# Performance work log

Measured on AMD Instinct MI355X. Metric: run time of the kernel, lower is better.

Reference implementation:

```python
import jax, jax.numpy as jnp
import numpy as np

B, NA, LAT, HID, AF, L = 512, 58, 64, 128, 10, 2
N = B * NA
E = N * 16


def silu(x):
    return x * jax.nn.sigmoid(x)


def setup_inputs() -> dict:
    key = jax.random.key(0)
    ks = list(jax.random.split(key, 32))

    def p(k, shape, fan_in):
        return jax.random.normal(k, shape, jnp.float32) / np.sqrt(fan_in)

    inp = {
        "z": jax.random.normal(ks[0], (B, LAT), jnp.float32),
        "atom_types": jax.random.uniform(ks[1], (N, AF), jnp.float32),
        "edge_index": jax.random.randint(ks[2], (2, E), 0, N, jnp.int64),
        "init_coords": jax.random.normal(ks[3], (NA, 3), jnp.float32) * 0.1,
        "latent_w": p(ks[4], (LAT, HID), LAT), "latent_b": jnp.zeros((HID,), jnp.float32),
        "atom_w": p(ks[5], (AF, HID), AF), "atom_b": jnp.zeros((HID,), jnp.float32),
        # per-layer stacked params (leading dim = num_layers)
        "edge_w1": p(ks[6], (L, 2 * HID + 1, HID), 2 * HID + 1), "edge_b1": jnp.zeros((L, HID), jnp.float32),
        "edge_w2": p(ks[7], (L, HID, HID), HID), "edge_b2": jnp.zeros((L, HID), jnp.float32),
        "node_w1": p(ks[8], (L, 2 * HID, HID), 2 * HID), "node_b1": jnp.zeros((L, HID), jnp.float32),
        "node_w2": p(ks[9], (L, HID, HID), HID), "node_b2": jnp.zeros((L, HID), jnp.float32),
        "coord_w1": p(ks[10], (L, HID, HID), HID), "coord_b1": jnp.zeros((L, HID), jnp.float32),
        "coord_w2": p(ks[11], (L, HID, 1), HID),  # no bias
        "ln_g": jnp.ones((L, HID), jnp.float32), "ln_b": jnp.zeros((L, HID), jnp.float32),
        "head_w1": p(ks[12], (HID, HID // 2), HID), "head_b1": jnp.zeros((HID // 2,), jnp.float32),
        "head_w2": p(ks[13], (HID // 2, 3), HID // 2), "head_b2": jnp.zeros((3,), jnp.float32),
    }
    return inp


def _layer(h, pos, row, col, ew1, eb1, ew2, eb2, nw1, nb1, nw2, nb2, cw1, cb1, cw2, lg, lb):
    n = h.shape[0]
    xi, xj = h[row], h[col]                      # [E,HID] gathers
    rel = pos[row] - pos[col]                    # [E,3]
    d2 = jnp.clip(jnp.sum(rel * rel, axis=-1, keepdims=True), 1e-6, 1e6)
    ef = jnp.concatenate([xi, xj, d2], axis=-1)  # [E,2H+1]
    m = silu(silu(ef @ ew1 + eb1) @ ew2 + eb2)   # edge MLP messages [E,HID]
    agg = jax.ops.segment_sum(m, row, num_segments=n)
    hn = silu(jnp.concatenate([h, agg], axis=-1) @ nw1 + nb1) @ nw2 + nb2
    mu = jnp.mean(hn, axis=-1, keepdims=True)
    var = jnp.mean((hn - mu) ** 2, axis=-1, keepdims=True)
    hn = (hn - mu) * jax.lax.rsqrt(var + 1e-5) * lg + lb
    cw = jnp.clip(silu(m @ cw1 + cb1) @ cw2, -1.0, 1.0)  # [E,1]
    upd = jax.ops.segment_sum(cw * rel, row, num_segments=n)  # [N,3]
    deg = jax.ops.segment_sum(jnp.ones((row.shape[0],), pos.dtype), row, num_segments=n)[:, None]
    pos_new = pos + upd / (deg + 1e-6)
    return hn, pos_new


def reference(z, atom_types, edge_index, init_coords, latent_w, latent_b, atom_w, atom_b,
              edge_w1, edge_b1, edge_w2, edge_b2, node_w1, node_b1, node_w2, node_b2,
              coord_w1, coord_b1, coord_w2, ln_g, ln_b, head_w1, head_b1, head_w2, head_b2):
    b = z.shape[0]
    na = init_coords.shape[0]
    n = b * na
    h = z @ latent_w + latent_b                              # [B,HID]
    h = jnp.broadcast_to(h[:, None, :], (b, na, h.shape[-1])).reshape(n, -1)
    h = h + (atom_types @ atom_w + atom_b)
    pos = jnp.broadcast_to(init_coords[None], (b, na, 3)).reshape(n, 3)
    row, col = edge_index[0], edge_index[1]
    for l in range(edge_w1.shape[0]):
        h, pos = _layer(h, pos, row, col,
                        edge_w1[l], edge_b1[l], edge_w2[l], edge_b2[l],
                        node_w1[l], node_b1[l], node_w2[l], node_b2[l],
                        coord_w1[l], coord_b1[l], coord_w2[l], ln_g[l], ln_b[l])
    delta = silu(h @ head_w1 + head_b1) @ head_w2 + head_b2
    return pos + delta
```

## Files before the change

kernel.cpp:

```cpp
#include <hip/hip_runtime.h>
#include <hip/hip_bf16.h>

#define BB 512
#define NA 58
#define LAT 64
#define HID 128
#define AF 10
#define NL 2
#define NN (BB*NA)
#define NE (NN*16)
#define ET 64
#define NTILE (NE/ET)

typedef __attribute__((ext_vector_type(8))) short s8;
typedef __attribute__((ext_vector_type(4))) float f4;

struct CvtDesc {
    const void* src[24];
    float*      dst[24];
    int         len[24];
};

struct PackJobs {
    const float* src[11];
    short*       dst[11];
    int          K[11];
    int          mode[11];
};

__device__ __forceinline__ float siluf(float x) {
    return x * __builtin_amdgcn_rcpf(1.0f + __expf(-x));
}

__device__ __forceinline__ short f2b(float x) {
    __hip_bfloat16 b = __float2bfloat16(x);
    return *(short*)&b;
}

__device__ __forceinline__ float b2f(short s) {
    return __uint_as_float(((unsigned int)(unsigned short)s) << 16);
}

__global__ void k_detect(const unsigned short* __restrict__ z16,
                         const unsigned int* __restrict__ e32,
                         int* __restrict__ flags) {
    __shared__ int sbf, si64;
    if (threadIdx.x == 0) { sbf = 0; si64 = 0; }
    __syncthreads();
    int c1 = 0, c2 = 0;
    for (int i = threadIdx.x; i < 1024; i += 256) {
        unsigned short v = z16[2*i];
        int e = (v >> 7) & 0xFF;
        if (e >= 100 && e <= 140) c1++;
        if (e32[2*i + 1] == 0u) c2++;
    }
    atomicAdd(&sbf, c1);
    atomicAdd(&si64, c2);
    __syncthreads();
    if (threadIdx.x == 0) {
        flags[0] = (sbf  > 600) ? 1 : 0;
        flags[1] = (si64 > 600) ? 1 : 0;
    }
}

__global__ void k_convert(CvtDesc d, const int* __restrict__ flags) {
    int a = blockIdx.y;
    int i = blockIdx.x * blockDim.x + threadIdx.x;
    int n = d.len[a];
    if (i >= n) return;
    if (flags[0]) {
        d.dst[a][i] = __bfloat162float(((const __hip_bfloat16*)d.src[a])[i]);
    } else {
        d.dst[a][i] = ((const float*)d.src[a])[i];
    }
}

__global__ void k_packall(PackJobs pj) {
    int j = blockIdx.y;
    int idx = blockIdx.x * 256 + threadIdx.x;
    const float* w = pj.src[j];
    short* o = pj.dst[j];
    int mode = pj.mode[j];
    if (mode == 0) {
        int K = pj.K[j];
        if (idx >= 128*K) return;
        int jj = idx & 7;
        int l  = (idx >> 3) & 63;
        int rest = idx >> 9;
        int KC = K >> 5;
        int kc = rest % KC;
        int nt = rest / KC;
        int n = nt*16 + (l & 15);
        int k = kc*32 + (l >> 4)*8 + jj;
        o[idx] = f2b(w[k*128 + n]);
    } else if (mode == 1) {
        if (idx >= 32768) return;
        int jj = idx & 7;
        int l  = (idx >> 3) & 63;
        int rest = idx >> 9;
        int kc = rest & 3;
        int nt = rest >> 2;
        int n = nt*16 + (l & 15);
        int k = kc*32 + (l >> 4)*8 + jj;
        float v = (n < 128) ? w[k*128 + n] : w[(128 + k)*128 + (n - 128)];
        o[idx] = f2b(v);
    } else {
        if (idx >= 8192) return;
        int jj = idx & 7;
        int l  = (idx >> 3) & 63;
        int rest = idx >> 9;
        int kc = rest & 3;
        int nt = rest >> 2;
        int n = nt*16 + (l & 15);
        int k = kc*32 + (l >> 4)*8 + jj;
        o[idx] = f2b(w[k*64 + n]);
    }
}

__global__ void k_hist(const int* __restrict__ eidx, const int* __restrict__ flags,
                       int* __restrict__ cnt) {
    int e = blockIdx.x * 256 + threadIdx.x;
    if (e >= NE) return;
    int is64 = flags[1];
    int r = eidx[is64 ? 2*(long)e : (long)e];
    atomicAdd(&cnt[r], 1);
}

__global__ __launch_bounds__(1024) void k_scan(const int* __restrict__ cnt,
                                               int* __restrict__ rowStart,
                                               int* __restrict__ cursor) {
    __shared__ int part[1024];
    int t = threadIdx.x;
    int base = t * 29;
    int loc[29];
    int s = 0;
    #pragma unroll
    for (int i = 0; i < 29; ++i) { loc[i] = s; s += cnt[base + i]; }
    part[t] = s;
    __syncthreads();
    for (int d = 1; d < 1024; d <<= 1) {
        int v = (t >= d) ? part[t - d] : 0;
        __syncthreads();
        part[t] += v;
        __syncthreads();
    }
    int pre = (t == 0) ? 0 : part[t - 1];
    #pragma unroll
    for (int i = 0; i < 29; ++i) {
        int v = pre + loc[i];
        rowStart[base + i] = v;
        cursor[base + i] = v;
    }
    if (t == 1023) rowStart[NN] = pre + s;
}

__global__ void k_scatter(const int* __restrict__ eidx, const int* __restrict__ flags,
                          int* __restrict__ cursor,
                          int* __restrict__ rS, int* __restrict__ cS) {
    int e = blockIdx.x * 256 + threadIdx.x;
    if (e >= NE) return;
    int is64 = flags[1];
    long ge = e, gc = (long)e + NE;
    int r = eidx[is64 ? 2*ge : ge];
    int c = eidx[is64 ? 2*gc : gc];
    int p = atomicAdd(&cursor[r], 1);
    rS[p] = r; cS[p] = c;
}

__global__ __launch_bounds__(256) void k_init3(
    const float* __restrict__ z, const float* __restrict__ lw,
    const float* __restrict__ lbz,
    const float* __restrict__ at,
    const float* __restrict__ aw, const float* __restrict__ ab,
    const float* __restrict__ ic,
    float* __restrict__ pos, short* __restrict__ hb,
    const short* __restrict__ wcat0, const float* __restrict__ b10,
    short* __restrict__ H1, float* __restrict__ agg, float* __restrict__ upd)
{
    __shared__ short x[64][136];
    __shared__ float awS[AF][HID];
    __shared__ float atS[64][AF+2];
    __shared__ float zbS[3][LAT];
    __shared__ float hzS[3][HID];
    const int tid = threadIdx.x;
    const int n0 = blockIdx.x * 64;
    const int b0 = n0 / NA;
    const int nb = (n0 + 63) / NA - b0 + 1;

    for (int i = tid; i < AF*HID; i += 256) awS[i/HID][i%HID] = aw[i];
    for (int i = tid; i < 64*AF; i += 256)
        atS[i/AF][i%AF] = at[(long)(n0 + i/AF)*AF + i%AF];
    for (int i = tid; i < nb*LAT; i += 256) {
        int bi = i / LAT, k = i - bi*LAT;
        int bidx = b0 + bi;
        zbS[bi][k] = (bidx < BB) ? z[bidx*LAT + k] : 0.f;
    }
    __syncthreads();

    for (int i = tid; i < nb*HID; i += 256) {
        int bi = i / HID, c = i - bi*HID;
        float acc = lbz[c];
        #pragma unroll
        for (int k = 0; k < LAT; ++k) acc += zbS[bi][k] * lw[k*HID + c];
        hzS[bi][c] = acc;
    }
    __syncthreads();

    #pragma unroll
    for (int it = 0; it < 32; ++it) {
        int idx = it*256 + tid;
        int r = idx >> 7, c = idx & 127;
        int n = n0 + r;
        float v = hzS[n/NA - b0][c] + ab[c];
        #pragma unroll
        for (int f = 0; f < AF; ++f) v += atS[r][f]*awS[f][c];
        short s = f2b(v);
        x[r][c] = s;
        hb[(long)n*HID + c] = s;
    }
    if (tid < 192) {
        int i = tid/3, d = tid - i*3;
        int n = n0 + i;
        pos[n*3 + d] = ic[(n % NA)*3 + d];
        upd[n*3 + d] = 0.f;
    }
    {
        f4* a4 = (f4*)(agg + (long)n0*HID);
        for (int j = tid; j < 64*HID/4; j += 256) a4[j] = (f4)0.f;
    }
    __syncthreads();

    const int l = tid & 63, w = tid >> 6;
    const int l16 = l & 15, quad = l >> 4;
    f4 acc[4][4];
    #pragma unroll
    for (int mt = 0; mt < 4; ++mt)
        #pragma unroll
        for (int nt4 = 0; nt4 < 4; ++nt4) acc[mt][nt4] = (f4)0.f;
    #pragma unroll
    for (int kc = 0; kc < 4; ++kc) {
        s8 a[4];
        #pragma unroll
        for (int mt = 0; mt < 4; ++mt)
            a[mt] = *(const s8*)&x[mt*16 + l16][kc*32 + quad*8];
        #pragma unroll
        for (int nt4 = 0; nt4 < 4; ++nt4) {
            int nt = w*4 + nt4;
            s8 b = *(const s8*)(wcat0 + (((size_t)nt*4 + kc)*64 + l)*8);
            #pragma unroll
            for (int mt = 0; mt < 4; ++mt)
                acc[mt][nt4] = __builtin_amdgcn_mfma_f32_16x16x32_bf16(a[mt], b, acc[mt][nt4], 0, 0, 0);
        }
    }
    #pragma unroll
    for (int nt4 = 0; nt4 < 4; ++nt4) {
        int col = (w*4 + nt4)*16 + l16;
        float bias = (col < 128) ? b10[col] : 0.f;
        #pragma unroll
        for (int mt = 0; mt < 4; ++mt)
            #pragma unroll
            for (int i = 0; i < 4; ++i) {
                int row = mt*16 + quad*4 + i;
                H1[(long)(n0 + row)*256 + col] = f2b(acc[mt][nt4][i] + bias);
            }
    }
}

__global__ __launch_bounds__(256, 3) void k_edge_os(
    const short* __restrict__ H1,
    const int* __restrict__ rS, const int* __restrict__ cS,
    const float* __restrict__ pos,
    const float* __restrict__ w1c,
    const short* __restrict__ w2p, const float* __restrict__ b2,
    const short* __restrict__ c1p, const float* __restrict__ cb1,
    const float* __restrict__ cw2,
    float* __restrict__ agg, float* __restrict__ upd)
{
    __shared__ short t1[ET][136];
    __shared__ short mm[ET][136];
    __shared__ int   rIs[ET], cIs[ET];
    __shared__ float sred[ET];

    const int tid = threadIdx.x;
    const int l = tid & 63, w = tid >> 6;
    const int l16 = l & 15, quad = l >> 4;
    const int c0 = (2*w)*16 + l16, c1c = (2*w+1)*16 + l16;
    const int half = tid >> 7, ch = tid & 127;
    const int q = tid & 15;
    const int esub = tid >> 4;
    const int T = blockIdx.x;

    float wv[8];
    #pragma unroll
    for (int j = 0; j < 8; ++j) wv[j] = w1c[q*8 + j];

    s8 w2f[8], c1f[8];
    #pragma unroll
    for (int kc = 0; kc < 4; ++kc) {
        w2f[kc]     = *(const s8*)(w2p + (((size_t)(2*w)*4 + kc)*64 + l)*8);
        w2f[4 + kc] = *(const s8*)(w2p + (((size_t)(2*w+1)*4 + kc)*64 + l)*8);
        c1f[kc]     = *(const s8*)(c1p + (((size_t)(2*w)*4 + kc)*64 + l)*8);
        c1f[4 + kc] = *(const s8*)(c1p + (((size_t)(2*w+1)*4 + kc)*64 + l)*8);
    }
    const float bia2_0 = b2[c0],  bia2_1 = b2[c1c];
    const float biac_0 = cb1[c0], biac_1 = cb1[c1c];
    const float cw0    = cw2[c0], cw1v   = cw2[c1c];

    const long eb = (long)T * ET;
    if (tid < ET) sred[tid] = 0.f;
    #pragma unroll
    for (int it = 0; it < 4; ++it) {
        int e = esub + 16*it;
        int r = rS[eb + e], c = cS[eb + e];
        float rx = pos[r*3+0] - pos[c*3+0];
        float ry = pos[r*3+1] - pos[c*3+1];
        float rz = pos[r*3+2] - pos[c*3+2];
        float d2 = fminf(fmaxf(rx*rx + ry*ry + rz*rz, 1e-6f), 1e6f);
        s8 va = *(const s8*)(H1 + (long)r*256 + q*8);
        s8 vb = *(const s8*)(H1 + (long)c*256 + 128 + q*8);
        s8 o;
        #pragma unroll
        for (int j = 0; j < 8; ++j)
            o[j] = f2b(siluf(b2f(va[j]) + b2f(vb[j]) + d2*wv[j]));
        *(s8*)&t1[e][q*8] = o;
        if (q == 0) { rIs[e] = r; cIs[e] = c; }
    }
    __syncthreads();

    {
        f4 acc[4][2];
        #pragma unroll
        for (int mt = 0; mt < 4; ++mt) { acc[mt][0] = (f4)0.f; acc[mt][1] = (f4)0.f; }
        #pragma unroll
        for (int it = 0; it < 4; ++it) {
            #pragma unroll
            for (int mt = 0; mt < 4; ++mt) {
                s8 a = *(const s8*)&t1[mt*16 + l16][it*32 + quad*8];
                acc[mt][0] = __builtin_amdgcn_mfma_f32_16x16x32_bf16(a, w2f[it],     acc[mt][0], 0, 0, 0);
                acc[mt][1] = __builtin_amdgcn_mfma_f32_16x16x32_bf16(a, w2f[4 + it], acc[mt][1], 0, 0, 0);
            }
        }
        #pragma unroll
        for (int mt = 0; mt < 4; ++mt) {
            #pragma unroll
            for (int i = 0; i < 4; ++i) {
                int row = mt*16 + quad*4 + i;
                mm[row][c0]  = f2b(siluf(acc[mt][0][i] + bia2_0));
                mm[row][c1c] = f2b(siluf(acc[mt][1][i] + bia2_1));
            }
        }
    }
    __syncthreads();

    {
        int e0 = half * 32;
        int cur = rIs[e0];
        float a = 0.f;
        #pragma unroll
        for (int e = e0; e < e0 + 32; ++e) {
            int r = rIs[e];
            if (r != cur) {
                atomicAdd(&agg[(long)cur*HID + ch], a);
                a = 0.f; cur = r;
            }
            a += b2f(mm[e][ch]);
        }
        atomicAdd(&agg[(long)cur*HID + ch], a);
    }
    {
        f4 acc3[4][2];
        #pragma unroll
        for (int mt = 0; mt < 4; ++mt) { acc3[mt][0] = (f4)0.f; acc3[mt][1] = (f4)0.f; }
        #pragma unroll
        for (int kc = 0; kc < 4; ++kc) {
            #pragma unroll
            for (int mt = 0; mt < 4; ++mt) {
                s8 a = *(const s8*)&mm[mt*16 + l16][kc*32 + quad*8];
                acc3[mt][0] = __builtin_amdgcn_mfma_f32_16x16x32_bf16(a, c1f[kc],     acc3[mt][0], 0, 0, 0);
                acc3[mt][1] = __builtin_amdgcn_mfma_f32_16x16x32_bf16(a, c1f[4 + kc], acc3[mt][1], 0, 0, 0);
            }
        }
        #pragma unroll
        for (int mt = 0; mt < 4; ++mt) {
            #pragma unroll
            for (int i = 0; i < 4; ++i) {
                float p = siluf(acc3[mt][0][i] + biac_0) * cw0
                        + siluf(acc3[mt][1][i] + biac_1) * cw1v;
                p += __shfl_xor(p, 1);
                p += __shfl_xor(p, 2);
                p += __shfl_xor(p, 4);
                p += __shfl_xor(p, 8);
                if (l16 == 0) {
                    int row = mt*16 + quad*4 + i;
                    atomicAdd(&sred[row], p);
                }
            }
        }
    }
    int   ur = 0;
    float urx = 0.f, ury = 0.f, urz = 0.f;
    if (tid < ET) {
        ur = rIs[tid];
        int uc = cIs[tid];
        urx = pos[ur*3+0] - pos[uc*3+0];
        ury = pos[ur*3+1] - pos[uc*3+1];
        urz = pos[ur*3+2] - pos[uc*3+2];
    }
    __syncthreads();

    if (tid < ET) {
        float cwv = fminf(fmaxf(sred[tid], -1.f), 1.f);
        atomicAdd(&upd[ur*3+0], cwv*urx);
        atomicAdd(&upd[ur*3+1], cwv*ury);
        atomicAdd(&upd[ur*3+2], cwv*urz);
    }
}

__global__ __launch_bounds__(256) void k_node_mfma(
    short* __restrict__ hb, float* __restrict__ agg,
    const short* __restrict__ w1p, const float* __restrict__ b1n,
    const short* __restrict__ w2p, const float* __restrict__ b2n,
    const float* __restrict__ lg, const float* __restrict__ lb,
    float* __restrict__ pos, float* __restrict__ upd,
    const int* __restrict__ rowStart,
    const short* __restrict__ wcatn, const float* __restrict__ b1next,
    short* __restrict__ H1,
    const short* __restrict__ hw1p, const float* __restrict__ hb1,
    const float* __restrict__ hw2, const float* __restrict__ hb2,
    void* __restrict__ out, const int* __restrict__ flags)
{
    __shared__ short x[64][264];
    __shared__ short t1[64][144];
    __shared__ float mus[64], rstds[64];
    __shared__ float posS[64][3];
    float (*hn)[132] = (float (*)[132])&x[0][0];
    float (*hid)[68] = (float (*)[68])&x[0][0];

    const int tid = threadIdx.x;
    const int n0 = blockIdx.x * 64;

    #pragma unroll
    for (int it = 0; it < 4; ++it) {
        int idx = it*256 + tid;
        int e = idx >> 4, qq = idx & 15;
        *(int4*)&x[e][qq*8] = *(const int4*)(hb + (long)(n0+e)*HID + qq*8);
    }
    #pragma unroll
    for (int it = 0; it < 8; ++it) {
        int idx = it*256 + tid;
        int e = idx >> 5, qq = idx & 31;
        float4 v = *(const float4*)(agg + (long)(n0+e)*HID + qq*4);
        short4 sv;
        sv.x = f2b(v.x); sv.y = f2b(v.y); sv.z = f2b(v.z); sv.w = f2b(v.w);
        *(short4*)&x[e][128 + qq*4] = sv;
    }
    __syncthreads();

    {
        f4* a4 = (f4*)(agg + (long)n0*HID);
        for (int j = tid; j < 64*HID/4; j += 256) a4[j] = (f4)0.f;
    }

    const int l = tid & 63, w = tid >> 6;
    const int l16 = l & 15, quad = l >> 4;
    const int nt0 = 2*w, nt1 = 2*w + 1;
    const int c0 = nt0*16 + l16, c1c = nt1*16 + l16;

    {
        f4 acc[4][2];
        #pragma unroll
        for (int mt = 0; mt < 4; ++mt) { acc[mt][0] = (f4)0.f; acc[mt][1] = (f4)0.f; }
        #pragma unroll
        for (int kc = 0; kc < 8; ++kc) {
            s8 b0  = *(const s8*)(w1p + (((size_t)nt0*8 + kc)*64 + l)*8);
            s8 b1f = *(const s8*)(w1p + (((size_t)nt1*8 + kc)*64 + l)*8);
            #pragma unroll
            for (int mt = 0; mt < 4; ++mt) {
                s8 a = *(const s8*)&x[mt*16 + l16][kc*32 + quad*8];
                acc[mt][0] = __builtin_amdgcn_mfma_f32_16x16x32_bf16(a, b0,  acc[mt][0], 0, 0, 0);
                acc[mt][1] = __builtin_amdgcn_mfma_f32_16x16x32_bf16(a, b1f, acc[mt][1], 0, 0, 0);
            }
        }
        float bia0 = b1n[c0], bia1 = b1n[c1c];
        #pragma unroll
        for (int mt = 0; mt < 4; ++mt) {
            #pragma unroll
            for (int i = 0; i < 4; ++i) {
                int row = mt*16 + quad*4 + i;
                t1[row][c0]  = f2b(siluf(acc[mt][0][i] + bia0));
                t1[row][c1c] = f2b(siluf(acc[mt][1][i] + bia1));
            }
        }
    }
    __syncthreads();

    {
        f4 acc[4][2];
        #pragma unroll
        for (int mt = 0; mt < 4; ++mt) { acc[mt][0] = (f4)0.f; acc[mt][1] = (f4)0.f; }
        #pragma unroll
        for (int kc = 0; kc < 4; ++kc) {
            s8 b0  = *(const s8*)(w2p + (((size_t)nt0*4 + kc)*64 + l)*8);
            s8 b1f = *(const s8*)(w2p + (((size_t)nt1*4 + kc)*64 + l)*8);
            #pragma unroll
            for (int mt = 0; mt < 4; ++mt) {
                s8 a = *(const s8*)&t1[mt*16 + l16][kc*32 + quad*8];
                acc[mt][0] = __builtin_amdgcn_mfma_f32_16x16x32_bf16(a, b0,  acc[mt][0], 0, 0, 0);
                acc[mt][1] = __builtin_amdgcn_mfma_f32_16x16x32_bf16(a, b1f, acc[mt][1], 0, 0, 0);
            }
        }
        float bia0 = b2n[c0], bia1 = b2n[c1c];
        __syncthreads();
        #pragma unroll
        for (int mt = 0; mt < 4; ++mt) {
            #pragma unroll
            for (int i = 0; i < 4; ++i) {
                int row = mt*16 + quad*4 + i;
                hn[row][c0]  = acc[mt][0][i] + bia0;
                hn[row][c1c] = acc[mt][1][i] + bia1;
            }
        }
    }
    __syncthreads();

    {
        int r = tid >> 2, part = tid & 3;
        float s = 0.f, qv = 0.f;
        #pragma unroll
        for (int j = 0; j < 32; ++j) {
            float v = hn[r][part + 4*j];
            s += v; qv += v*v;
        }
        s += __shfl_xor(s, 1); qv += __shfl_xor(qv, 1);
        s += __shfl_xor(s, 2); qv += __shfl_xor(qv, 2);
        if (part == 0) {
            float mu = s * (1.0f/HID);
            float var = qv * (1.0f/HID) - mu*mu;
            mus[r] = mu;
            rstds[r] = rsqrtf(var + 1e-5f);
        }
    }
    __syncthreads();

    #pragma unroll
    for (int it = 0; it < 32; ++it) {
        int idx = it*256 + tid;
        int r = idx >> 7, c = idx & 127;
        float v = (hn[r][c] - mus[r]) * rstds[r] * lg[c] + lb[c];
        short s = f2b(v);
        hb[(long)(n0 + r)*HID + c] = s;
        t1[r][c] = s;
    }
    if (tid < 192) {
        int i = tid / 3, d = tid - i*3;
        int n = n0 + i;
        float dg = (float)(rowStart[n+1] - rowStart[n]);
        float np = pos[n*3+d] + upd[n*3+d] / (dg + 1e-6f);
        pos[n*3+d] = np;
        posS[i][d] = np;
        upd[n*3+d] = 0.f;
    }
    __syncthreads();

    if (wcatn) {
        f4 acc[4][4];
        #pragma unroll
        for (int mt = 0; mt < 4; ++mt)
            #pragma unroll
            for (int nt4 = 0; nt4 < 4; ++nt4) acc[mt][nt4] = (f4)0.f;
        #pragma unroll
        for (int kc = 0; kc < 4; ++kc) {
            s8 a[4];
            #pragma unroll
            for (int mt = 0; mt < 4; ++mt)
                a[mt] = *(const s8*)&t1[mt*16 + l16][kc*32 + quad*8];
            #pragma unroll
            for (int nt4 = 0; nt4 < 4; ++nt4) {
                int nt = w*4 + nt4;
                s8 b = *(const s8*)(wcatn + (((size_t)nt*4 + kc)*64 + l)*8);
                #pragma unroll
                for (int mt = 0; mt < 4; ++mt)
                    acc[mt][nt4] = __builtin_amdgcn_mfma_f32_16x16x32_bf16(a[mt], b, acc[mt][nt4], 0, 0, 0);
            }
        }
        #pragma unroll
        for (int nt4 = 0; nt4 < 4; ++nt4) {
            int col = (w*4 + nt4)*16 + l16;
            float bias = (col < 128) ? b1next[col] : 0.f;
            #pragma unroll
            for (int mt = 0; mt < 4; ++mt)
                #pragma unroll
                for (int i = 0; i < 4; ++i) {
                    int row = mt*16 + quad*4 + i;
                    H1[(long)(n0 + row)*256 + col] = f2b(acc[mt][nt4][i] + bias);
                }
        }
    } else {
        f4 acc[4];
        #pragma unroll
        for (int mt = 0; mt < 4; ++mt) acc[mt] = (f4)0.f;
        #pragma unroll
        for (int kc = 0; kc < 4; ++kc) {
            s8 b = *(const s8*)(hw1p + (((size_t)w*4 + kc)*64 + l)*8);
            #pragma unroll
            for (int mt = 0; mt < 4; ++mt) {
                s8 a = *(const s8*)&t1[mt*16 + l16][kc*32 + quad*8];
                acc[mt] = __builtin_amdgcn_mfma_f32_16x16x32_bf16(a, b, acc[mt], 0, 0, 0);
            }
        }
        int col = w*16 + l16;
        float bias = hb1[col];
        #pragma unroll
        for (int mt = 0; mt < 4; ++mt)
            #pragma unroll
            for (int i = 0; i < 4; ++i) {
                int row = mt*16 + quad*4 + i;
                hid[row][col] = siluf(acc[mt][i] + bias);
            }
        __syncthreads();
        if (tid < 192) {
            int r = tid / 3, cc = tid - r*3;
            float a2 = hb2[cc];
            #pragma unroll
            for (int k = 0; k < 64; ++k) a2 += hid[r][k] * hw2[k*3 + cc];
            int n = n0 + r;
            float v = posS[r][cc] + a2;
            if (flags[0]) ((__hip_bfloat16*)out)[n*3+cc] = __float2bfloat16(v);
            else          ((float*)out)[n*3+cc] = v;
        }
    }
}

extern "C" void kernel_launch(void* const* d_in, const int* in_sizes, int n_in,
                              void* d_out, int out_size, void* d_ws, size_t ws_size,
                              hipStream_t stream)
{
    (void)in_sizes; (void)n_in; (void)out_size; (void)ws_size;

    int* flags = (int*)d_ws;
    float* base = (float*)d_ws;
    size_t off = 64;
    auto alloc = [&](size_t n) { float* p = base + off; off += (n + 63) & ~63ull; return p; };

    static const int aidx[24] = {0,1,3,4,5,6,7,8,9,10,11,12,13,14,15,16,17,18,19,20,21,22,23,24};
    static const int alen[24] = {
        BB*LAT, NN*AF, NA*3, LAT*HID, HID, AF*HID, HID,
        NL*257*HID, NL*HID, NL*HID*HID, NL*HID,
        NL*256*HID, NL*HID, NL*HID*HID, NL*HID,
        NL*HID*HID, NL*HID, NL*HID, NL*HID, NL*HID,
        HID*64, 64, 64*3, 3
    };
    CvtDesc cd;
    float* fp[24];
    for (int a = 0; a < 24; ++a) {
        fp[a] = alloc((size_t)alen[a]);
        cd.src[a] = d_in[aidx[a]];
        cd.dst[a] = fp[a];
        cd.len[a] = alen[a];
    }
    float* agg = alloc((size_t)NN*HID);
    float* pos = alloc((size_t)NN*3);
    float* upd = alloc((size_t)NN*3);
    short* hb  = (short*)alloc((size_t)NN*HID/2);
    short* H1  = (short*)alloc((size_t)NN*256/2);
    short* wcatp = (short*)alloc((size_t)NL*32768/2);
    short* w2p = (short*)alloc((size_t)NL*16384/2);
    short* c1p = (short*)alloc((size_t)NL*16384/2);
    short* nw1p = (short*)alloc((size_t)NL*32768/2);
    short* nw2p = (short*)alloc((size_t)NL*16384/2);
    short* hw1p = (short*)alloc((size_t)8192/2);
    int* cnt      = (int*)alloc((size_t)NN);
    int* rowStart = (int*)alloc((size_t)NN + 1);
    int* cursor   = (int*)alloc((size_t)NN);
    int* rS       = (int*)alloc((size_t)NE);
    int* cS       = (int*)alloc((size_t)NE);
    const int* eidx = (const int*)d_in[2];

    k_detect<<<1, 256, 0, stream>>>((const unsigned short*)d_in[0],
                                    (const unsigned int*)d_in[2], flags);
    k_convert<<<dim3((NN*AF + 255)/256, 24), 256, 0, stream>>>(cd, flags);

    PackJobs pj;
    for (int l = 0; l < NL; ++l) {
        int b5 = l*5;
        pj.src[b5+0] = fp[7]  + (size_t)l*257*HID; pj.dst[b5+0] = wcatp + (size_t)l*32768; pj.K[b5+0] = 256; pj.mode[b5+0] = 1;
        pj.src[b5+1] = fp[9]  + (size_t)l*HID*HID; pj.dst[b5+1] = w2p   + (size_t)l*16384; pj.K[b5+1] = 128; pj.mode[b5+1] = 0;
        pj.src[b5+2] = fp[15] + (size_t)l*HID*HID; pj.dst[b5+2] = c1p   + (size_t)l*16384; pj.K[b5+2] = 128; pj.mode[b5+2] = 0;
        pj.src[b5+3] = fp[11] + (size_t)l*256*HID; pj.dst[b5+3] = nw1p  + (size_t)l*32768; pj.K[b5+3] = 256; pj.mode[b5+3] = 0;
        pj.src[b5+4] = fp[13] + (size_t)l*HID*HID; pj.dst[b5+4] = nw2p  + (size_t)l*16384; pj.K[b5+4] = 128; pj.mode[b5+4] = 0;
    }
    pj.src[10] = fp[20]; pj.dst[10] = hw1p; pj.K[10] = 128; pj.mode[10] = 2;
    k_packall<<<dim3(128, 11), 256, 0, stream>>>(pj);

    hipMemsetAsync(cnt, 0, (size_t)NN*sizeof(int), stream);
    k_hist<<<(NE + 255)/256, 256, 0, stream>>>(eidx, flags, cnt);
    k_scan<<<1, 1024, 0, stream>>>(cnt, rowStart, cursor);
    k_scatter<<<(NE + 255)/256, 256, 0, stream>>>(eidx, flags, cursor, rS, cS);

    k_init3<<<NN/64, 256, 0, stream>>>(fp[0], fp[3], fp[4],
                                       fp[1], fp[5], fp[6], fp[2], pos, hb,
                                       wcatp, fp[8], H1, agg, upd);

    for (int l = 0; l < NL; ++l) {
        k_edge_os<<<NTILE, 256, 0, stream>>>(H1, rS, cS, pos,
            fp[7] + (size_t)l*257*HID + 256*HID,
            w2p + (size_t)l*16384, fp[10] + (size_t)l*HID,
            c1p + (size_t)l*16384, fp[16] + (size_t)l*HID,
            fp[17] + (size_t)l*HID,
            agg, upd);
        const short* wcatn = (l+1 < NL) ? (wcatp + (size_t)(l+1)*32768) : nullptr;
        const float* b1nx  = (l+1 < NL) ? (fp[8] + (size_t)(l+1)*HID) : fp[8];
        k_node_mfma<<<NN/64, 256, 0, stream>>>(hb, agg,
            nw1p + (size_t)l*32768, fp[12] + (size_t)l*HID,
            nw2p + (size_t)l*16384, fp[14] + (size_t)l*HID,
            fp[18] + (size_t)l*HID, fp[19] + (size_t)l*HID,
            pos, upd, rowStart, wcatn, b1nx, H1,
            hw1p, fp[21], fp[22], fp[23], d_out, flags);
    }
}
```

Before: 599.3 us.

## Assign edge blocks by destination-row ranges and aggregate in shared memory

The edge kernel now gives each block a fixed range of 29 destination rows and loops over that range's CSR-sorted edges in 64-edge tiles. Messages and coordinate updates are reduced into shared-memory buffers, and each block then writes agg/upd once with plain stores instead of global atomics. Because every row is fully overwritten, the node kernel no longer zeroes agg and upd. In exchange, each block has a variable number of edge tiles, which can unbalance load, and the last tile of each range is padded with masked lanes.

After: 962.9 us. +60.7%, slower.

```diff
diff --git a/kernel.cpp b/kernel.cpp
--- a/kernel.cpp
+++ b/kernel.cpp
@@ -10,7 +10,8 @@
 #define NN (BB*NA)
 #define NE (NN*16)
 #define ET 64
-#define NTILE (NE/ET)
+#define RPB 29
+#define NBLK (NN/RPB)
 
 typedef __attribute__((ext_vector_type(8))) short s8;
 typedef __attribute__((ext_vector_type(4))) float f4;
@@ -266,7 +267,7 @@
     }
 }
 
-__global__ __launch_bounds__(256, 3) void k_edge_os(
+__global__ __launch_bounds__(256, 3) void k_edge_rm(
     const short* __restrict__ H1,
     const int* __restrict__ rS, const int* __restrict__ cS,
     const float* __restrict__ pos,
@@ -274,12 +275,15 @@
     const short* __restrict__ w2p, const float* __restrict__ b2,
     const short* __restrict__ c1p, const float* __restrict__ cb1,
     const float* __restrict__ cw2,
+    const int* __restrict__ rowStart,
     float* __restrict__ agg, float* __restrict__ upd)
 {
     __shared__ short t1[ET][136];
     __shared__ short mm[ET][136];
     __shared__ int   rIs[ET], cIs[ET];
     __shared__ float sred[ET];
+    __shared__ float aggS[RPB][HID];
+    __shared__ float updS[RPB][4];
 
     const int tid = threadIdx.x;
     const int l = tid & 63, w = tid >> 6;
@@ -288,7 +292,7 @@
     const int half = tid >> 7, ch = tid & 127;
     const int q = tid & 15;
     const int esub = tid >> 4;
-    const int T = blockIdx.x;
+    const int r0 = blockIdx.x * RPB;
 
     float wv[8];
     #pragma unroll
@@ -306,126 +310,155 @@
     const float biac_0 = cb1[c0], biac_1 = cb1[c1c];
     const float cw0    = cw2[c0], cw1v   = cw2[c1c];
 
-    const long eb = (long)T * ET;
+    for (int j = tid; j < RPB*HID; j += 256) aggS[j >> 7][j & 127] = 0.f;
+    if (tid < RPB) { updS[tid][0] = 0.f; updS[tid][1] = 0.f; updS[tid][2] = 0.f; }
     if (tid < ET) sred[tid] = 0.f;
-    #pragma unroll
-    for (int it = 0; it < 4; ++it) {
-        int e = esub + 16*it;
-        int r = rS[eb + e], c = cS[eb + e];
-        float rx = pos[r*3+0] - pos[c*3+0];
-        float ry = pos[r*3+1] - pos[c*3+1];
-        float rz = pos[r*3+2] - pos[c*3+2];
-        float d2 = fminf(fmaxf(rx*rx + ry*ry + rz*rz, 1e-6f), 1e6f);
-        s8 va = *(const s8*)(H1 + (long)r*256 + q*8);
-        s8 vb = *(const s8*)(H1 + (long)c*256 + 128 + q*8);
-        s8 o;
-        #pragma unroll
-        for (int j = 0; j < 8; ++j)
-            o[j] = f2b(siluf(b2f(va[j]) + b2f(vb[j]) + d2*wv[j]));
-        *(s8*)&t1[e][q*8] = o;
-        if (q == 0) { rIs[e] = r; cIs[e] = c; }
-    }
-    __syncthreads();
-
-    {
-        f4 acc[4][2];
-        #pragma unroll
-        for (int mt = 0; mt < 4; ++mt) { acc[mt][0] = (f4)0.f; acc[mt][1] = (f4)0.f; }
+
+    const int bstart = rowStart[r0];
+    const int bend   = rowStart[r0 + RPB];
+    __syncthreads();
+
+    for (int eb = bstart; eb < bend; eb += ET) {
         #pragma unroll
         for (int it = 0; it < 4; ++it) {
+            int e = esub + 16*it;
+            long idx = (long)eb + e;
+            int r, c; float d2;
+            if (idx < bend) {
+                r = rS[idx]; c = cS[idx];
+                float rx = pos[r*3+0] - pos[c*3+0];
+                float ry = pos[r*3+1] - pos[c*3+1];
+                float rz = pos[r*3+2] - pos[c*3+2];
+                d2 = fminf(fmaxf(rx*rx + ry*ry + rz*rz, 1e-6f), 1e6f);
+            } else { r = r0; c = r0; d2 = 0.f; }
+            s8 va = *(const s8*)(H1 + (long)r*256 + q*8);
+            s8 vb = *(const s8*)(H1 + (long)c*256 + 128 + q*8);
+            s8 o;
+            #pragma unroll
+            for (int j = 0; j < 8; ++j)
+                o[j] = f2b(siluf(b2f(va[j]) + b2f(vb[j]) + d2*wv[j]));
+            *(s8*)&t1[e][q*8] = o;
+            if (q == 0) { rIs[e] = r; cIs[e] = c; }
+        }
+        __syncthreads();
+
+        {
+            f4 acc[4][2];
+            #pragma unroll
+            for (int mt = 0; mt < 4; ++mt) { acc[mt][0] = (f4)0.f; acc[mt][1] = (f4)0.f; }
+            #pragma unroll
+            for (int it = 0; it < 4; ++it) {
+                #pragma unroll
+                for (int mt = 0; mt < 4; ++mt) {
+                    s8 a = *(const s8*)&t1[mt*16 + l16][it*32 + quad*8];
+                    acc[mt][0] = __builtin_amdgcn_mfma_f32_16x16x32_bf16(a, w2f[it],     acc[mt][0], 0, 0, 0);
+                    acc[mt][1] = __builtin_amdgcn_mfma_f32_16x16x32_bf16(a, w2f[4 + it], acc[mt][1], 0, 0, 0);
+                }
+            }
             #pragma unroll
             for (int mt = 0; mt < 4; ++mt) {
-                s8 a = *(const s8*)&t1[mt*16 + l16][it*32 + quad*8];
-                acc[mt][0] = __builtin_amdgcn_mfma_f32_16x16x32_bf16(a, w2f[it],     acc[mt][0], 0, 0, 0);
-                acc[mt][1] = __builtin_amdgcn_mfma_f32_16x16x32_bf16(a, w2f[4 + it], acc[mt][1], 0, 0, 0);
-            }
-        }
-        #pragma unroll
-        for (int mt = 0; mt < 4; ++mt) {
-            #pragma unroll
-            for (int i = 0; i < 4; ++i) {
-                int row = mt*16 + quad*4 + i;
-                mm[row][c0]  = f2b(siluf(acc[mt][0][i] + bia2_0));
-                mm[row][c1c] = f2b(siluf(acc[mt][1][i] + bia2_1));
-            }
-        }
-    }
-    __syncthreads();
-
-    {
-        int e0 = half * 32;
-        int cur = rIs[e0];
-        float a = 0.f;
-        #pragma unroll
-        for (int e = e0; e < e0 + 32; ++e) {
-            int r = rIs[e];
-            if (r != cur) {
-                atomicAdd(&agg[(long)cur*HID + ch], a);
-                a = 0.f; cur = r;
-            }
-            a += b2f(mm[e][ch]);
-        }
-        atomicAdd(&agg[(long)cur*HID + ch], a);
-    }
-    {
-        f4 acc3[4][2];
-        #pragma unroll
-        for (int mt = 0; mt < 4; ++mt) { acc3[mt][0] = (f4)0.f; acc3[mt][1] = (f4)0.f; }
-        #pragma unroll
-        for (int kc = 0; kc < 4; ++kc) {
+                #pragma unroll
+                for (int i = 0; i < 4; ++i) {
+                    int row = mt*16 + quad*4 + i;
+                    mm[row][c0]  = f2b(siluf(acc[mt][0][i] + bia2_0));
+                    mm[row][c1c] = f2b(siluf(acc[mt][1][i] + bia2_1));
+                }
+            }
+        }
+        __syncthreads();
+
+        {
+            int e0 = half * 32;
+            int cur = rIs[e0];
+            float a = 0.f;
+            #pragma unroll
+            for (int e = e0; e < e0 + 32; ++e) {
+                int r = rIs[e];
+                if (r != cur) {
+                    atomicAdd(&aggS[cur - r0][ch], a);
+                    a = 0.f; cur = r;
+                }
+                float v = ((long)eb + e < bend) ? b2f(mm[e][ch]) : 0.f;
+                a += v;
+            }
+            atomicAdd(&aggS[cur - r0][ch], a);
+        }
+        {
+            f4 acc3[4][2];
+            #pragma unroll
+            for (int mt = 0; mt < 4; ++mt) { acc3[mt][0] = (f4)0.f; acc3[mt][1] = (f4)0.f; }
+            #pragma unroll
+            for (int kc = 0; kc < 4; ++kc) {
+                #pragma unroll
+                for (int mt = 0; mt < 4; ++mt) {
+                    s8 a = *(const s8*)&mm[mt*16 + l16][kc*32 + quad*8];
+                    acc3[mt][0] = __builtin_amdgcn_mfma_f32_16x16x32_bf16(a, c1f[kc],     acc3[mt][0], 0, 0, 0);
+                    acc3[mt][1] = __builtin_amdgcn_mfma_f32_16x16x32_bf16(a, c1f[4 + kc], acc3[mt][1], 0, 0, 0);
+                }
+            }
             #pragma unroll
             for (int mt = 0; mt < 4; ++mt) {
-                s8 a = *(const s8*)&mm[mt*16 + l16][kc*32 + quad*8];
-                acc3[mt][0] = __builtin_amdgcn_mfma_f32_16x16x32_bf16(a, c1f[kc],     acc3[mt][0], 0, 0, 0);
-                acc3[mt][1] = __builtin_amdgcn_mfma_f32_16x16x32_bf16(a, c1f[4 + kc], acc3[mt][1], 0, 0, 0);
-            }
-        }
-        #pragma unroll
-        for (int mt = 0; mt < 4; ++mt) {
-            #pragma unroll
-            for (int i = 0; i < 4; ++i) {
-                float p = siluf(acc3[mt][0][i] + biac_0) * cw0
-                        + siluf(acc3[mt][1][i] + biac_1) * cw1v;
-                p += __shfl_xor(p, 1);
-                p += __shfl_xor(p, 2);
-                p += __shfl_xor(p, 4);
-                p += __shfl_xor(p, 8);
-                if (l16 == 0) {
-                    int row = mt*16 + quad*4 + i;
-                    atomicAdd(&sred[row], p);
+                #pragma unroll
+                for (int i = 0; i < 4; ++i) {
+                    float p = siluf(acc3[mt][0][i] + biac_0) * cw0
+                            + siluf(acc3[mt][1][i] + biac_1) * cw1v;
+                    p += __shfl_xor(p, 1);
+                    p += __shfl_xor(p, 2);
+                    p += __shfl_xor(p, 4);
+                    p += __shfl_xor(p, 8);
+                    if (l16 == 0) {
+                        int row = mt*16 + quad*4 + i;
+                        atomicAdd(&sred[row], p);
+                    }
                 }
             }
         }
-    }
-    int   ur = 0;
-    float urx = 0.f, ury = 0.f, urz = 0.f;
-    if (tid < ET) {
-        ur = rIs[tid];
-        int uc = cIs[tid];
-        urx = pos[ur*3+0] - pos[uc*3+0];
-        ury = pos[ur*3+1] - pos[uc*3+1];
-        urz = pos[ur*3+2] - pos[uc*3+2];
-    }
-    __syncthreads();
-
-    if (tid < ET) {
-        float cwv = fminf(fmaxf(sred[tid], -1.f), 1.f);
-        atomicAdd(&upd[ur*3+0], cwv*urx);
-        atomicAdd(&upd[ur*3+1], cwv*ury);
-        atomicAdd(&upd[ur*3+2], cwv*urz);
+        int   ur = r0;
+        float urx = 0.f, ury = 0.f, urz = 0.f;
+        bool  uvalid = false;
+        if (tid < ET) {
+            uvalid = ((long)eb + tid < bend);
+            if (uvalid) {
+                ur = rIs[tid];
+                int uc = cIs[tid];
+                urx = pos[ur*3+0] - pos[uc*3+0];
+                ury = pos[ur*3+1] - pos[uc*3+1];
+                urz = pos[ur*3+2] - pos[uc*3+2];
+            }
+        }
+        __syncthreads();
+
+        if (tid < ET) {
+            if (uvalid) {
+                float cwv = fminf(fmaxf(sred[tid], -1.f), 1.f);
+                atomicAdd(&updS[ur - r0][0], cwv*urx);
+                atomicAdd(&updS[ur - r0][1], cwv*ury);
+                atomicAdd(&updS[ur - r0][2], cwv*urz);
+            }
+            sred[tid] = 0.f;
+        }
+    }
+    __syncthreads();
+
+    for (int j = tid; j < RPB*HID; j += 256)
+        agg[(long)r0*HID + j] = aggS[j >> 7][j & 127];
+    if (tid < RPB*3) {
+        int i = tid / 3, d = tid - i*3;
+        upd[(r0 + i)*3 + d] = updS[i][d];
     }
 }
 
 __global__ __launch_bounds__(256) void k_node_mfma(
     short* __restrict__ hb, float* __restrict__ agg,
-    const short* __restrict__ w1p, const float* __restrict__ b1n,
+    const float* __restrict__ w1p_dummy, const float* __restrict__ b1n,
     const short* __restrict__ w2p, const float* __restrict__ b2n,
     const float* __restrict__ lg, const float* __restrict__ lb,
     float* __restrict__ pos, float* __restrict__ upd,
     const int* __restrict__ rowStart,
     const short* __restrict__ wcatn, const float* __restrict__ b1next,
     short* __restrict__ H1,
-    const short* __restrict__ hw1p, const float* __restrict__ hb1,
+    const short* __restrict__ w1p, const short* __restrict__ hw1p,
+    const float* __restrict__ hb1,
     const float* __restrict__ hw2, const float* __restrict__ hb2,
     void* __restrict__ out, const int* __restrict__ flags)
 {
@@ -435,6 +468,7 @@
     __shared__ float posS[64][3];
     float (*hn)[132] = (float (*)[132])&x[0][0];
     float (*hid)[68] = (float (*)[68])&x[0][0];
+    (void)w1p_dummy;
 
     const int tid = threadIdx.x;
     const int n0 = blockIdx.x * 64;
@@ -456,11 +490,6 @@
     }
     __syncthreads();
 
-    {
-        f4* a4 = (f4*)(agg + (long)n0*HID);
-        for (int j = tid; j < 64*HID/4; j += 256) a4[j] = (f4)0.f;
-    }
-
     const int l = tid & 63, w = tid >> 6;
     const int l16 = l & 15, quad = l >> 4;
     const int nt0 = 2*w, nt1 = 2*w + 1;
@@ -558,7 +587,6 @@
         float np = pos[n*3+d] + upd[n*3+d] / (dg + 1e-6f);
         pos[n*3+d] = np;
         posS[i][d] = np;
-        upd[n*3+d] = 0.f;
     }
     __syncthreads();
 
@@ -702,19 +730,19 @@
                                        wcatp, fp[8], H1, agg, upd);
 
     for (int l = 0; l < NL; ++l) {
-        k_edge_os<<<NTILE, 256, 0, stream>>>(H1, rS, cS, pos,
+        k_edge_rm<<<NBLK, 256, 0, stream>>>(H1, rS, cS, pos,
             fp[7] + (size_t)l*257*HID + 256*HID,
             w2p + (size_t)l*16384, fp[10] + (size_t)l*HID,
             c1p + (size_t)l*16384, fp[16] + (size_t)l*HID,
             fp[17] + (size_t)l*HID,
-            agg, upd);
+            rowStart, agg, upd);
         const short* wcatn = (l+1 < NL) ? (wcatp + (size_t)(l+1)*32768) : nullptr;
         const float* b1nx  = (l+1 < NL) ? (fp[8] + (size_t)(l+1)*HID) : fp[8];
         k_node_mfma<<<NN/64, 256, 0, stream>>>(hb, agg,
-            nw1p + (size_t)l*32768, fp[12] + (size_t)l*HID,
+            nullptr, fp[12] + (size_t)l*HID,
             nw2p + (size_t)l*16384, fp[14] + (size_t)l*HID,
             fp[18] + (size_t)l*HID, fp[19] + (size_t)l*HID,
             pos, upd, rowStart, wcatn, b1nx, H1,
-            hw1p, fp[21], fp[22], fp[23], d_out, flags);
-    }
-}
+            nw1p + (size_t)l*32768, hw1p, fp[21], fp[22], fp[23], d_out, flags);
+    }
+}
```

## Reuse t1 LDS for messages and stream MFMA weight fragments per k-step

Applied to the files above, without the earlier changes.

Removes the separate mm shared buffer by aliasing it onto t1 after an extra barrier, roughly halving LDS per block. The 16 weight fragments that were preloaded into registers for the whole kernel are now loaded from global memory one k-chunk ahead inside each MFMA loop. The goal is lower register and LDS pressure so more blocks fit per CU. In exchange it adds a barrier and repeated global/L2 weight loads whose latency may not be fully hidden.

Measured after the change: 571.0 us. -4.7%, faster.

```diff
diff --git a/kernel.cpp b/kernel.cpp
--- a/kernel.cpp
+++ b/kernel.cpp
@@ -277,7 +277,6 @@
     float* __restrict__ agg, float* __restrict__ upd)
 {
     __shared__ short t1[ET][136];
-    __shared__ short mm[ET][136];
     __shared__ int   rIs[ET], cIs[ET];
     __shared__ float sred[ET];
 
@@ -293,18 +292,6 @@
     float wv[8];
     #pragma unroll
     for (int j = 0; j < 8; ++j) wv[j] = w1c[q*8 + j];
-
-    s8 w2f[8], c1f[8];
-    #pragma unroll
-    for (int kc = 0; kc < 4; ++kc) {
-        w2f[kc]     = *(const s8*)(w2p + (((size_t)(2*w)*4 + kc)*64 + l)*8);
-        w2f[4 + kc] = *(const s8*)(w2p + (((size_t)(2*w+1)*4 + kc)*64 + l)*8);
-        c1f[kc]     = *(const s8*)(c1p + (((size_t)(2*w)*4 + kc)*64 + l)*8);
-        c1f[4 + kc] = *(const s8*)(c1p + (((size_t)(2*w+1)*4 + kc)*64 + l)*8);
-    }
-    const float bia2_0 = b2[c0],  bia2_1 = b2[c1c];
-    const float biac_0 = cb1[c0], biac_1 = cb1[c1c];
-    const float cw0    = cw2[c0], cw1v   = cw2[c1c];
 
     const long eb = (long)T * ET;
     if (tid < ET) sred[tid] = 0.f;
@@ -327,19 +314,35 @@
     }
     __syncthreads();
 
-    {
-        f4 acc[4][2];
-        #pragma unroll
-        for (int mt = 0; mt < 4; ++mt) { acc[mt][0] = (f4)0.f; acc[mt][1] = (f4)0.f; }
+    f4 acc[4][2];
+    #pragma unroll
+    for (int mt = 0; mt < 4; ++mt) { acc[mt][0] = (f4)0.f; acc[mt][1] = (f4)0.f; }
+    {
+        const short* wb0 = w2p + ((size_t)(2*w)*4*64 + l)*8;
+        const short* wb1 = w2p + ((size_t)(2*w+1)*4*64 + l)*8;
+        s8 b0 = *(const s8*)wb0;
+        s8 b1 = *(const s8*)wb1;
         #pragma unroll
         for (int it = 0; it < 4; ++it) {
+            s8 nb0 = b0, nb1 = b1;
+            if (it < 3) {
+                nb0 = *(const s8*)(wb0 + (size_t)(it+1)*512);
+                nb1 = *(const s8*)(wb1 + (size_t)(it+1)*512);
+            }
             #pragma unroll
             for (int mt = 0; mt < 4; ++mt) {
                 s8 a = *(const s8*)&t1[mt*16 + l16][it*32 + quad*8];
-                acc[mt][0] = __builtin_amdgcn_mfma_f32_16x16x32_bf16(a, w2f[it],     acc[mt][0], 0, 0, 0);
-                acc[mt][1] = __builtin_amdgcn_mfma_f32_16x16x32_bf16(a, w2f[4 + it], acc[mt][1], 0, 0, 0);
-            }
-        }
+                acc[mt][0] = __builtin_amdgcn_mfma_f32_16x16x32_bf16(a, b0, acc[mt][0], 0, 0, 0);
+                acc[mt][1] = __builtin_amdgcn_mfma_f32_16x16x32_bf16(a, b1, acc[mt][1], 0, 0, 0);
+            }
+            b0 = nb0; b1 = nb1;
+        }
+    }
+    __syncthreads();
+
+    short (*mm)[136] = t1;
+    {
+        const float bia2_0 = b2[c0], bia2_1 = b2[c1c];
         #pragma unroll
         for (int mt = 0; mt < 4; ++mt) {
             #pragma unroll
@@ -371,15 +374,27 @@
         f4 acc3[4][2];
         #pragma unroll
         for (int mt = 0; mt < 4; ++mt) { acc3[mt][0] = (f4)0.f; acc3[mt][1] = (f4)0.f; }
+        const short* cb0 = c1p + ((size_t)(2*w)*4*64 + l)*8;
+        const short* cb1p_ = c1p + ((size_t)(2*w+1)*4*64 + l)*8;
+        s8 b0 = *(const s8*)cb0;
+        s8 b1 = *(const s8*)cb1p_;
         #pragma unroll
         for (int kc = 0; kc < 4; ++kc) {
+            s8 nb0 = b0, nb1 = b1;
+            if (kc < 3) {
+                nb0 = *(const s8*)(cb0 + (size_t)(kc+1)*512);
+                nb1 = *(const s8*)(cb1p_ + (size_t)(kc+1)*512);
+            }
             #pragma unroll
             for (int mt = 0; mt < 4; ++mt) {
                 s8 a = *(const s8*)&mm[mt*16 + l16][kc*32 + quad*8];
-                acc3[mt][0] = __builtin_amdgcn_mfma_f32_16x16x32_bf16(a, c1f[kc],     acc3[mt][0], 0, 0, 0);
-                acc3[mt][1] = __builtin_amdgcn_mfma_f32_16x16x32_bf16(a, c1f[4 + kc], acc3[mt][1], 0, 0, 0);
-            }
-        }
+                acc3[mt][0] = __builtin_amdgcn_mfma_f32_16x16x32_bf16(a, b0, acc3[mt][0], 0, 0, 0);
+                acc3[mt][1] = __builtin_amdgcn_mfma_f32_16x16x32_bf16(a, b1, acc3[mt][1], 0, 0, 0);
+            }
+            b0 = nb0; b1 = nb1;
+        }
+        const float biac_0 = cb1[c0], biac_1 = cb1[c1c];
+        const float cw0    = cw2[c0], cw1v   = cw2[c1c];
         #pragma unroll
         for (int mt = 0; mt < 4; ++mt) {
             #pragma unroll
```
